# Kernel optimization log

Hardware: AMD Instinct MI355X
Metric: run time of the kernel (lower is better)

The kernel has to match this reference:

```python
import jax, jax.numpy as jnp
import numpy as np

B, S, D, H = 64, 256, 2048, 8
DH = D // H  # 256; NOTE: S must equal DH for the original module's broadcast to be valid
EPS = 1e-06


def setup_inputs() -> dict:
    key = jax.random.key(0)
    ks = jax.random.split(key, 8)
    s = 1.0 / np.sqrt(D)
    x = jax.random.normal(ks[0], (B, S, D), jnp.float32)
    Wq = jax.random.normal(ks[1], (D, D), jnp.float32) * s
    Wk = jax.random.normal(ks[2], (D, D), jnp.float32) * s
    Wv = jax.random.normal(ks[3], (D, D), jnp.float32) * s
    Wo = jax.random.normal(ks[4], (2 * D, D), jnp.float32) * (1.0 / np.sqrt(2 * D))
    bq = jnp.zeros((D,), jnp.float32)
    bk = jnp.zeros((D,), jnp.float32)
    bv = jnp.zeros((D,), jnp.float32)
    bo = jnp.zeros((D,), jnp.float32)
    gamma = jnp.ones((D,), jnp.float32)
    beta = jnp.zeros((D,), jnp.float32)
    return {"x": x, "Wq": Wq, "bq": bq, "Wk": Wk, "bk": bk, "Wv": Wv, "bv": bv,
            "Wo": Wo, "bo": bo, "gamma": gamma, "beta": beta}


def reference(x, Wq, bq, Wk, bk, Wv, bv, Wo, bo, gamma, beta):
    def split_heads(t):  # [B,S,D] -> [B,H,S,DH]
        return t.reshape(B, S, H, DH).transpose(0, 2, 1, 3)

    q_proj = x @ Wq + bq  # reused later as the residual projection
    q = jax.nn.elu(split_heads(q_proj)) + 1.0
    k = jax.nn.elu(split_heads(x @ Wk + bk)) + 1.0
    v = split_heads(x @ Wv + bv)

    key_sum = k.sum(axis=2, keepdims=True)  # [B,H,1,DH]
    # Original TF code broadcasts [B,H,S,S] / [B,H,1,DH]; valid because S == DH
    scores = jnp.einsum('bhqd,bhkd->bhqk', q, k) / (key_sum + EPS)
    attn = jnp.einsum('bhqk,bhkd->bhqd', scores, v)
    attn = attn.transpose(0, 2, 1, 3).reshape(B, S, D)

    summary = jnp.broadcast_to(attn.mean(axis=1, keepdims=True), (B, S, D))
    combined = jnp.concatenate([attn, summary], axis=-1) @ Wo + bo  # [B,S,D]
    # dropout is identity (training=False)

    z = q_proj + combined
    mu = z.mean(axis=-1, keepdims=True)
    var = z.var(axis=-1, keepdims=True)
    return (z - mu) / jnp.sqrt(var + EPS) * gamma + beta
```

## Files before the change

### kernel.cpp

```cpp
#include <hip/hip_runtime.h>
#include <hip/hip_bf16.h>

typedef __attribute__((ext_vector_type(8))) __bf16 bf16x8v;
typedef __attribute__((ext_vector_type(4))) float f32x4;
typedef __attribute__((ext_vector_type(4))) unsigned short u16x4;
typedef __attribute__((ext_vector_type(8))) unsigned short u16x8;

#define LN_EPS 1e-6f

__device__ __forceinline__ unsigned short f2bf(float f) {
  union { float f; unsigned int u; } v; v.f = f;
  unsigned int r = v.u + 0x7fffu + ((v.u >> 16) & 1u);
  return (unsigned short)(r >> 16);
}
__device__ __forceinline__ float bf2f(unsigned short u) {
  union { unsigned int u; float f; } v; v.u = ((unsigned int)u) << 16;
  return v.f;
}
__device__ __forceinline__ float elu1(float x) {
  return x > 0.f ? x + 1.f : __expf(x);
}
__device__ __forceinline__ void gload16(const void* g, void* l) {
  __builtin_amdgcn_global_load_lds((__attribute__((address_space(1))) void*)g,
                                   (__attribute__((address_space(3))) void*)l,
                                   16, 0, 0);
}

__global__ __launch_bounds__(256) void cvt_f32_bf16(const float* __restrict__ in,
                                                    unsigned short* __restrict__ out, long n) {
  long stride = (long)gridDim.x * 256 * 8;
  for (long i = ((long)blockIdx.x * 256 + threadIdx.x) * 8; i < n; i += stride) {
    float4 a = *(const float4*)(in + i);
    float4 b = *(const float4*)(in + i + 4);
    u16x8 o;
    o[0] = f2bf(a.x); o[1] = f2bf(a.y); o[2] = f2bf(a.z); o[3] = f2bf(a.w);
    o[4] = f2bf(b.x); o[5] = f2bf(b.y); o[6] = f2bf(b.z); o[7] = f2bf(b.w);
    *(u16x8*)(out + i) = o;
  }
}

__global__ __launch_bounds__(256) void tr_cvt(const float* __restrict__ in,
                                              unsigned short* __restrict__ out, int R, int C) {
  __shared__ float t[64][65];
  int r0 = blockIdx.y * 64, c0 = blockIdx.x * 64;
  for (int idx = threadIdx.x; idx < 4096; idx += 256) {
    int r = idx >> 6, c = idx & 63;
    t[r][c] = in[(long)(r0 + r) * C + c0 + c];
  }
  __syncthreads();
  for (int idx = threadIdx.x; idx < 4096; idx += 256) {
    int c = idx >> 6, r = idx & 63;
    out[(long)(c0 + c) * R + r0 + r] = f2bf(t[r][c]);
  }
}

__global__ __launch_bounds__(256) void colsum_bf16(const unsigned short* __restrict__ in,
                                                   float* __restrict__ out, int rows, float scale) {
  int b = blockIdx.y;
  int col = blockIdx.x * 256 + threadIdx.x;
  const unsigned short* p = in + (long)b * rows * 2048 + col;
  float acc = 0.f;
  for (int s = 0; s < rows; ++s) acc += bf2f(p[(long)s * 2048]);
  out[(long)b * 2048 + col] = acc * scale;
}

__global__ __launch_bounds__(256) void srow_part(const float* __restrict__ summ,
                                                 const float* __restrict__ Wo2,
                                                 float* __restrict__ part) {
  int col = blockIdx.x * 256 + threadIdx.x;
  int b = blockIdx.y;
  int k0 = blockIdx.z * 256;
  const float* s = summ + (long)b * 2048 + k0;
  const float* w = Wo2 + (long)k0 * 2048 + col;
  float acc = 0.f;
#pragma unroll 8
  for (int k = 0; k < 256; ++k) acc += s[k] * w[(long)k * 2048];
  part[((long)blockIdx.z * 64 + b) * 2048 + col] = acc;
}
__global__ __launch_bounds__(256) void srow_sum(const float* __restrict__ part,
                                                float* __restrict__ srow) {
  int col = blockIdx.x * 256 + threadIdx.x;
  int b = blockIdx.y;
  float acc = 0.f;
#pragma unroll
  for (int kb = 0; kb < 8; ++kb) acc += part[((long)kb * 64 + b) * 2048 + col];
  srow[(long)b * 2048 + col] = acc;
}

__global__ __launch_bounds__(256) void ln_k(const unsigned short* __restrict__ z,
                                            const float* __restrict__ gamma,
                                            const float* __restrict__ beta,
                                            float* __restrict__ out) {
  long row = blockIdx.x;
  int t = threadIdx.x;
  u16x8 zv = *(const u16x8*)(z + row * 2048 + t * 8);
  float zf[8];
  float s = 0.f, q = 0.f;
#pragma unroll
  for (int j = 0; j < 8; ++j) {
    zf[j] = bf2f(zv[j]);
    s += zf[j];
    q += zf[j] * zf[j];
  }
#pragma unroll
  for (int o = 32; o >= 1; o >>= 1) { s += __shfl_xor(s, o); q += __shfl_xor(q, o); }
  __shared__ float ss[4], qq[4];
  if ((t & 63) == 0) { ss[t >> 6] = s; qq[t >> 6] = q; }
  __syncthreads();
  s = ss[0] + ss[1] + ss[2] + ss[3];
  q = qq[0] + qq[1] + qq[2] + qq[3];
  float mu = s * (1.f / 2048.f);
  float var = q * (1.f / 2048.f) - mu * mu;
  float rstd = rsqrtf(var + LN_EPS);
  float4 g1 = *(const float4*)(gamma + t * 8);
  float4 g2 = *(const float4*)(gamma + t * 8 + 4);
  float4 b1 = *(const float4*)(beta + t * 8);
  float4 b2 = *(const float4*)(beta + t * 8 + 4);
  float4 o1, o2;
  o1.x = (zf[0] - mu) * rstd * g1.x + b1.x;
  o1.y = (zf[1] - mu) * rstd * g1.y + b1.y;
  o1.z = (zf[2] - mu) * rstd * g1.z + b1.z;
  o1.w = (zf[3] - mu) * rstd * g1.w + b1.w;
  o2.x = (zf[4] - mu) * rstd * g2.x + b2.x;
  o2.y = (zf[5] - mu) * rstd * g2.y + b2.y;
  o2.z = (zf[6] - mu) * rstd * g2.z + b2.z;
  o2.w = (zf[7] - mu) * rstd * g2.w + b2.w;
  *(float4*)(out + row * 2048 + t * 8) = o1;
  *(float4*)(out + row * 2048 + t * 8 + 4) = o2;
}

struct GemmArgs {
  const unsigned short* A; long lda, sAb, sAh;
  const unsigned short* B; long ldb, sBb, sBh;
  char* C; long ldc, sCb, sCh;
  int K;
  const float* aux; long sXb, sXh;
  const unsigned short* residb;
  const float* srow;
  unsigned short* out2;
  const float* bk2;
  const float* bv2;
  unsigned short* kact2;
  unsigned short* vt2;
};

template <int EPI>
__device__ __forceinline__ void epi_frag(const GemmArgs& g, char* Cb, int bz, int hz,
                                         long grow0, long gcol, f32x4 v) {
  if (EPI == 6) {
    const int wsel = (int)(gcol >> 11);
    const long cw = gcol & 2047;
    if (wsel == 0) {
      const float bias = g.aux[cw];
      unsigned short* Ch = (unsigned short*)Cb;
#pragma unroll
      for (int rr = 0; rr < 4; ++rr) {
        const long idx = (grow0 + rr) * 2048 + cw;
        const float vv = v[rr] + bias;
        Ch[idx] = f2bf(vv);
        g.out2[idx] = f2bf(elu1(vv));
      }
    } else if (wsel == 1) {
      const float bias = g.bk2[cw];
#pragma unroll
      for (int rr = 0; rr < 4; ++rr)
        g.kact2[(grow0 + rr) * 2048 + cw] = f2bf(elu1(v[rr] + bias));
    } else {
      const float bias = g.bv2[cw];
      const long batch = grow0 >> 8;
      const int sloc = (int)(grow0 & 255);
      u16x4 pk;
#pragma unroll
      for (int rr = 0; rr < 4; ++rr) pk[rr] = f2bf(v[rr] + bias);
      *(u16x4*)(g.vt2 + (batch * 2048 + cw) * 256 + sloc) = pk;
    }
  } else if (EPI == 3) {
    const float* divs = g.aux + bz * g.sXb + hz * g.sXh;
    const float d = divs[gcol] + LN_EPS;
    unsigned short* Ch = (unsigned short*)Cb;
#pragma unroll
    for (int rr = 0; rr < 4; ++rr)
      Ch[(grow0 + rr) * g.ldc + gcol] = f2bf(v[rr] / d);
  } else if (EPI == 4) {
    unsigned short* Ch = (unsigned short*)Cb;
#pragma unroll
    for (int rr = 0; rr < 4; ++rr)
      Ch[(grow0 + rr) * g.ldc + gcol] = f2bf(v[rr]);
  } else {
    const float bias = g.aux[gcol];
    unsigned short* Ch = (unsigned short*)Cb;
#pragma unroll
    for (int rr = 0; rr < 4; ++rr) {
      const long grow = grow0 + rr;
      const long idx = grow * g.ldc + gcol;
      const float vv = v[rr] + bias + bf2f(g.residb[idx]) + g.srow[(grow >> 8) * 2048 + gcol];
      Ch[idx] = f2bf(vv);
    }
  }
}

template <int EPI>
__global__ __launch_bounds__(256, 4) void gemm_bt(GemmArgs g) {
  const int tid = threadIdx.x;
  const int lane = tid & 63;
  const int wave = tid >> 6;
  const int wm = wave >> 1, wn = wave & 1;
  const int bz = (int)blockIdx.z >> 3, hz = (int)blockIdx.z & 7;
  const long mBase = (long)blockIdx.x * 128;
  const long nBase = (long)blockIdx.y * 128;
  const unsigned short* Ab = g.A + bz * g.sAb + hz * g.sAh;
  const unsigned short* Bb = g.B + bz * g.sBb + hz * g.sBh;

  __shared__ __align__(16) unsigned short Asm[128 * 64];
  __shared__ __align__(16) unsigned short Bsm[128 * 64];

  f32x4 acc[4][4] = {};

  for (int kt = 0; kt < g.K; kt += 64) {
#pragma unroll
    for (int i = 0; i < 4; ++i) {
      const int u = i * 256 + tid;
      const int rr = u >> 3;
      const int cc = (((u & 7) ^ (rr & 7)) << 3);
      gload16(Ab + (mBase + rr) * g.lda + kt + cc, Asm + (size_t)u * 8);
      gload16(Bb + (nBase + rr) * g.ldb + kt + cc, Bsm + (size_t)u * 8);
    }
    __syncthreads();
#pragma unroll
    for (int ks = 0; ks < 64; ks += 32) {
      const int kof = ks + ((lane >> 4) << 3);
      bf16x8v a[4], b[4];
#pragma unroll
      for (int mi = 0; mi < 4; ++mi) {
        const int row = wm * 64 + mi * 16 + (lane & 15);
        a[mi] = *(const bf16x8v*)&Asm[row * 64 + (kof ^ ((row & 7) << 3))];
      }
#pragma unroll
      for (int ni = 0; ni < 4; ++ni) {
        const int row = wn * 64 + ni * 16 + (lane & 15);
        b[ni] = *(const bf16x8v*)&Bsm[row * 64 + (kof ^ ((row & 7) << 3))];
      }
#pragma unroll
      for (int mi = 0; mi < 4; ++mi)
#pragma unroll
        for (int ni = 0; ni < 4; ++ni)
          acc[mi][ni] = __builtin_amdgcn_mfma_f32_16x16x32_bf16(a[mi], b[ni], acc[mi][ni], 0, 0, 0);
    }
    __syncthreads();
  }

  char* Cb = g.C + bz * g.sCb + hz * g.sCh;
#pragma unroll
  for (int mi = 0; mi < 4; ++mi) {
    const long grow0 = mBase + wm * 64 + mi * 16 + ((lane >> 4) << 2);
#pragma unroll
    for (int ni = 0; ni < 4; ++ni)
      epi_frag<EPI>(g, Cb, bz, hz, grow0, nBase + wn * 64 + ni * 16 + (lane & 15), acc[mi][ni]);
  }
}

extern "C" void kernel_launch(void* const* d_in, const int* in_sizes, int n_in,
                              void* d_out, int out_size, void* d_ws, size_t ws_size,
                              hipStream_t stream) {
  (void)in_sizes; (void)n_in; (void)out_size;
  const float* x     = (const float*)d_in[0];
  const float* Wq    = (const float*)d_in[1];
  const float* bq    = (const float*)d_in[2];
  const float* Wk    = (const float*)d_in[3];
  const float* bk    = (const float*)d_in[4];
  const float* Wv    = (const float*)d_in[5];
  const float* bv    = (const float*)d_in[6];
  const float* Wo    = (const float*)d_in[7];
  const float* bo    = (const float*)d_in[8];
  const float* gamma = (const float*)d_in[9];
  const float* beta  = (const float*)d_in[10];
  float* out = (float*)d_out;

  const long M = 16384, D = 2048;
  char* ws = (char*)d_ws;
  size_t o = 0;
  unsigned short* xbf = (unsigned short*)(ws + o); o += (size_t)M * D * 2;
  unsigned short* wqT = (unsigned short*)(ws + o); o += (size_t)D * D * 2;
  unsigned short* wkT = (unsigned short*)(ws + o); o += (size_t)D * D * 2;
  unsigned short* wvT = (unsigned short*)(ws + o); o += (size_t)D * D * 2;
  unsigned short* woT = (unsigned short*)(ws + o); o += (size_t)D * D * 2;
  unsigned short* qpro = (unsigned short*)(ws + o); o += (size_t)M * D * 2;
  unsigned short* qact = (unsigned short*)(ws + o); o += (size_t)M * D * 2;
  unsigned short* kact = (unsigned short*)(ws + o); o += (size_t)M * D * 2;
  unsigned short* vT   = (unsigned short*)(ws + o); o += (size_t)M * D * 2;
  unsigned short* P    = (unsigned short*)(ws + o); o += (size_t)512 * 65536 * 2;
  float* ksum = (float*)(ws + o); o += (size_t)64 * 2048 * 4;
  float* summ = (float*)(ws + o); o += (size_t)64 * 2048 * 4;
  float* srow = (float*)(ws + o); o += (size_t)64 * 2048 * 4;
  unsigned short* attn = xbf;
  float* spart = (float*)P;
  if (ws_size < o) return;

  cvt_f32_bf16<<<2048, 256, 0, stream>>>(x, xbf, M * D);
  tr_cvt<<<dim3(32, 32), 256, 0, stream>>>(Wq, wqT, 2048, 2048);
  tr_cvt<<<dim3(32, 32), 256, 0, stream>>>(Wk, wkT, 2048, 2048);
  tr_cvt<<<dim3(32, 32), 256, 0, stream>>>(Wv, wvT, 2048, 2048);
  tr_cvt<<<dim3(32, 32), 256, 0, stream>>>(Wo, woT, 2048, 2048);

  GemmArgs a{};
  a.A = xbf; a.lda = 2048; a.sAb = 0; a.sAh = 0;
  a.B = wqT; a.ldb = 2048; a.sBb = 0; a.sBh = 0;
  a.C = (char*)qpro; a.ldc = 2048; a.sCb = 0; a.sCh = 0;
  a.K = 2048; a.aux = bq; a.sXb = 0; a.sXh = 0;
  a.residb = nullptr; a.srow = nullptr; a.out2 = qact;
  a.bk2 = bk; a.bv2 = bv; a.kact2 = kact; a.vt2 = vT;
  gemm_bt<6><<<dim3(128, 48, 1), 256, 0, stream>>>(a);

  colsum_bf16<<<dim3(8, 64), 256, 0, stream>>>(kact, ksum, 256, 1.0f);

  GemmArgs sA{};
  sA.A = qact; sA.lda = 2048; sA.sAb = 256 * 2048; sA.sAh = 256;
  sA.B = kact; sA.ldb = 2048; sA.sBb = 256 * 2048; sA.sBh = 256;
  sA.C = (char*)P; sA.ldc = 256; sA.sCb = 8L * 65536 * 2; sA.sCh = 65536L * 2;
  sA.K = 256; sA.aux = ksum; sA.sXb = 2048; sA.sXh = 256;
  sA.residb = nullptr; sA.srow = nullptr; sA.out2 = nullptr;
  gemm_bt<3><<<dim3(2, 2, 512), 256, 0, stream>>>(sA);

  GemmArgs tA{};
  tA.A = P; tA.lda = 256; tA.sAb = 8L * 65536; tA.sAh = 65536;
  tA.B = vT; tA.ldb = 256; tA.sBb = 2048L * 256; tA.sBh = 256 * 256;
  tA.C = (char*)attn; tA.ldc = 2048; tA.sCb = 256L * 2048 * 2; tA.sCh = 256 * 2;
  tA.K = 256; tA.aux = nullptr; tA.sXb = 0; tA.sXh = 0;
  tA.residb = nullptr; tA.srow = nullptr; tA.out2 = nullptr;
  gemm_bt<4><<<dim3(2, 2, 512), 256, 0, stream>>>(tA);

  colsum_bf16<<<dim3(8, 64), 256, 0, stream>>>(attn, summ, 256, 1.0f / 256.0f);
  srow_part<<<dim3(8, 64, 8), 256, 0, stream>>>(summ, Wo + (size_t)2048 * 2048, spart);
  srow_sum<<<dim3(8, 64), 256, 0, stream>>>(spart, srow);

  GemmArgs zA{};
  zA.A = attn; zA.lda = 2048; zA.sAb = 0; zA.sAh = 0;
  zA.B = woT; zA.ldb = 2048; zA.sBb = 0; zA.sBh = 0;
  zA.C = (char*)qpro; zA.ldc = 2048; zA.sCb = 0; zA.sCh = 0;
  zA.K = 2048; zA.aux = bo; zA.sXb = 0; zA.sXh = 0;
  zA.residb = qpro; zA.srow = srow; zA.out2 = nullptr;
  gemm_bt<5><<<dim3(128, 16, 1), 256, 0, stream>>>(zA);

  ln_k<<<16384, 256, 0, stream>>>(qpro, gamma, beta, out);
}
```

Before: 1.043 ms.

## Batch weight transposes into one launch and swizzle GEMM block order for XCD locality

```diff
diff --git a/kernel.cpp b/kernel.cpp
--- a/kernel.cpp
+++ b/kernel.cpp
@@ -39,18 +39,20 @@
   }
 }
 
-__global__ __launch_bounds__(256) void tr_cvt(const float* __restrict__ in,
-                                              unsigned short* __restrict__ out, int R, int C) {
+struct Tr4Args { const float* src[4]; unsigned short* dst[4]; };
+__global__ __launch_bounds__(256) void tr_cvt4(Tr4Args t4) {
   __shared__ float t[64][65];
+  const float* in = t4.src[blockIdx.z];
+  unsigned short* out = t4.dst[blockIdx.z];
   int r0 = blockIdx.y * 64, c0 = blockIdx.x * 64;
   for (int idx = threadIdx.x; idx < 4096; idx += 256) {
     int r = idx >> 6, c = idx & 63;
-    t[r][c] = in[(long)(r0 + r) * C + c0 + c];
+    t[r][c] = in[(long)(r0 + r) * 2048 + c0 + c];
   }
   __syncthreads();
   for (int idx = threadIdx.x; idx < 4096; idx += 256) {
     int c = idx >> 6, r = idx & 63;
-    out[(long)(c0 + c) * R + r0 + r] = f2bf(t[r][c]);
+    out[(long)(c0 + c) * 2048 + r0 + r] = f2bf(t[r][c]);
   }
 }
 
@@ -206,8 +208,20 @@
   const int wave = tid >> 6;
   const int wm = wave >> 1, wn = wave & 1;
   const int bz = (int)blockIdx.z >> 3, hz = (int)blockIdx.z & 7;
-  const long mBase = (long)blockIdx.x * 128;
-  const long nBase = (long)blockIdx.y * 128;
+
+  long mBase, nBase;
+  if (EPI == 3 || EPI == 4) {
+    mBase = (long)blockIdx.x * 128;
+    nBase = (long)blockIdx.y * 128;
+  } else {
+    const int nwg = (int)(gridDim.x * gridDim.y);
+    const int cpx = nwg >> 3;
+    const int lin = (int)blockIdx.y * (int)gridDim.x + (int)blockIdx.x;
+    const int swz = (lin & 7) * cpx + (lin >> 3);
+    mBase = (long)(swz % (int)gridDim.x) * 128;
+    nBase = (long)(swz / (int)gridDim.x) * 128;
+  }
+
   const unsigned short* Ab = g.A + bz * g.sAb + hz * g.sAh;
   const unsigned short* Bb = g.B + bz * g.sBb + hz * g.sBh;
 
@@ -297,10 +311,10 @@
   if (ws_size < o) return;
 
   cvt_f32_bf16<<<2048, 256, 0, stream>>>(x, xbf, M * D);
-  tr_cvt<<<dim3(32, 32), 256, 0, stream>>>(Wq, wqT, 2048, 2048);
-  tr_cvt<<<dim3(32, 32), 256, 0, stream>>>(Wk, wkT, 2048, 2048);
-  tr_cvt<<<dim3(32, 32), 256, 0, stream>>>(Wv, wvT, 2048, 2048);
-  tr_cvt<<<dim3(32, 32), 256, 0, stream>>>(Wo, woT, 2048, 2048);
+  Tr4Args t4;
+  t4.src[0] = Wq; t4.src[1] = Wk; t4.src[2] = Wv; t4.src[3] = Wo;
+  t4.dst[0] = wqT; t4.dst[1] = wkT; t4.dst[2] = wvT; t4.dst[3] = woT;
+  tr_cvt4<<<dim3(32, 32, 4), 256, 0, stream>>>(t4);
 
   GemmArgs a{};
   a.A = xbf; a.lda = 2048; a.sAb = 0; a.sAh = 0;
```

Measured after the change: 1.209 ms. 1.16x slower.
